# Performance work log

Measured on AMD Instinct MI355X. Metric: run time of the kernel, lower is better.

Reference implementation:

```python
import jax, jax.numpy as jnp
import numpy as np

VOCAB, EMB, HID = 50000, 256, 512
N, T = 256, 512


def setup_inputs() -> dict:
    key = jax.random.key(0)
    ks = jax.random.split(key, 9)
    s_ih = 1.0 / np.sqrt(HID)
    return {
        "input1": jax.random.randint(ks[0], (N, T), 0, VOCAB, dtype=jnp.int32),
        "input2": jax.random.randint(ks[1], (N, T), 0, VOCAB, dtype=jnp.int32),
        "emb_table": jax.random.normal(ks[2], (VOCAB, EMB), jnp.float32),
        "W_ih": jax.random.normal(ks[3], (4 * HID, EMB), jnp.float32) * s_ih,
        "W_hh": jax.random.normal(ks[4], (4 * HID, HID), jnp.float32) * s_ih,
        "b_ih": jax.random.normal(ks[5], (4 * HID,), jnp.float32) * s_ih,
        "b_hh": jax.random.normal(ks[6], (4 * HID,), jnp.float32) * s_ih,
        "W_fc": jax.random.normal(ks[7], (2, HID), jnp.float32) * s_ih,
        "b_fc": jax.random.normal(ks[8], (2,), jnp.float32) * s_ih,
    }


def _lstm_last_h(tokens, emb_table, W_ih, W_hh, b):
    # tokens: [N, T] int -> embedded [N, T, E]
    x = emb_table[tokens]
    # precompute input projections for all timesteps: [T, N, 4H]
    xg = jnp.einsum("nte,ge->tng", x, W_ih) + b
    h0 = jnp.zeros((tokens.shape[0], HID), x.dtype)
    c0 = jnp.zeros_like(h0)

    def step(carry, xg_t):
        h, c = carry
        gates = xg_t + h @ W_hh.T  # [N, 4H]
        i, f, g, o = jnp.split(gates, 4, axis=-1)
        i, f, o = jax.nn.sigmoid(i), jax.nn.sigmoid(f), jax.nn.sigmoid(o)
        g = jnp.tanh(g)
        c = f * c + i * g
        h = o * jnp.tanh(c)
        return (h, c), None

    (h, _), _ = jax.lax.scan(step, (h0, c0), xg)
    return h  # [N, HID]


def reference(input1, input2, emb_table, W_ih, W_hh, b_ih, b_hh, W_fc, b_fc):
    b = b_ih + b_hh
    h1 = _lstm_last_h(input1, emb_table, W_ih, W_hh, b)
    h2 = _lstm_last_h(input2, emb_table, W_ih, W_hh, b)
    h = h1 * h2  # combo_unit == 'MULT'
    logits = h @ W_fc.T + b_fc  # [N, 2]
    return jax.nn.softmax(logits, axis=1)
```

## Files before the change

kernel.cpp:

```cpp
#include <hip/hip_runtime.h>
#include <stdint.h>

#define VOCAB  50000
#define EMBD   256
#define HIDD   512
#define G4     2048
#define NBAT   256
#define TSEQ   512

#define O_P2    0ull
#define O_EMBT  204800000ull
#define O_WIH   230400000ull
#define O_WHH   231448576ull
#define O_TOKT  233545728ull
#define O_HBUF  234594304ull
#define O_BAR   235642880ull
#define WS_NEED 235643136ull
#define O_FLAGS O_EMBT

typedef __bf16 bf16x8 __attribute__((ext_vector_type(8)));
typedef float  f32x4  __attribute__((ext_vector_type(4)));
typedef float  f32x16 __attribute__((ext_vector_type(16)));

__device__ __forceinline__ unsigned short f2bf(float x) {
  unsigned u = __float_as_uint(x);
  u = (u + 0x7fffu + ((u >> 16) & 1u)) >> 16;
  return (unsigned short)u;
}
__device__ __forceinline__ float b2f(unsigned short b) {
  return __uint_as_float(((unsigned)b) << 16);
}
__device__ __forceinline__ float sigf(float x) {
  float e = __builtin_amdgcn_exp2f(-1.4426950408889634f * x);
  return __builtin_amdgcn_rcpf(1.0f + e);
}
__device__ __forceinline__ float tanhf_(float x) {
  float e = __builtin_amdgcn_exp2f(-2.8853900817779268f * x);
  return 2.0f * __builtin_amdgcn_rcpf(1.0f + e) - 1.0f;
}

__global__ void k_prep(const float* __restrict__ emb, const float* __restrict__ wih,
                       const float* __restrict__ whh, const int* __restrict__ tok1,
                       const int* __restrict__ tok2, unsigned short* __restrict__ embT,
                       unsigned short* __restrict__ wihb, unsigned short* __restrict__ whhb,
                       int* __restrict__ tokT, unsigned* __restrict__ hz)
{
  const int stride = gridDim.x * blockDim.x;
  const int id0 = blockIdx.x * blockDim.x + threadIdx.x;
  for (int i = id0; i < VOCAB * EMBD; i += stride) embT[i] = f2bf(emb[i]);
  for (int i = id0; i < G4 * EMBD; i += stride)    wihb[i] = f2bf(wih[i]);
  for (int i = id0; i < G4 * HIDD; i += stride)    whhb[i] = f2bf(whh[i]);
  for (int i = id0; i < 2 * TSEQ * NBAT; i += stride) {
    int l = i >> 17, t = (i >> 8) & 511, n = i & 255;
    tokT[i] = (l ? tok2 : tok1)[n * TSEQ + t];
  }
  for (int i = id0; i < 262144; i += stride) hz[i] = 0u;
}

__global__ void k_zero(unsigned* __restrict__ flags)
{
  const int i = blockIdx.x * blockDim.x + threadIdx.x;
  if (i < 16384) flags[i] = 0u;
}

__global__ __launch_bounds__(256) void
k_proj(const unsigned short* __restrict__ embT, const unsigned short* __restrict__ wihb,
       const float* __restrict__ bih, const float* __restrict__ bhh,
       unsigned short* __restrict__ P2)
{
  const int l  = threadIdx.x & 63;
  const int w  = threadIdx.x >> 6;
  const int n0 = blockIdx.x * 128 + (w & 1) * 64;
  const int m0 = blockIdx.y * 128 + (w >> 1) * 64;
  const int lq = l >> 4, lc = l & 15;

  f32x4 acc[4][4];
  #pragma unroll
  for (int a = 0; a < 4; ++a)
    #pragma unroll
    for (int b = 0; b < 4; ++b) acc[a][b] = (f32x4){0.f, 0.f, 0.f, 0.f};

  const uint8_t* eb = (const uint8_t*)embT;
  const uint8_t* wb = (const uint8_t*)wihb;
  #pragma unroll
  for (int ks = 0; ks < 8; ++ks) {
    const int koff = ks * 64 + lq * 16;
    bf16x8 a[4], b[4];
    #pragma unroll
    for (int mt = 0; mt < 4; ++mt) {
      int row = m0 + mt * 16 + lc; if (row >= VOCAB) row = VOCAB - 1;
      a[mt] = *(const bf16x8*)(eb + (size_t)row * 512 + koff);
    }
    #pragma unroll
    for (int nt = 0; nt < 4; ++nt) {
      int g = n0 + nt * 16 + lc;
      b[nt] = *(const bf16x8*)(wb + (size_t)g * 512 + koff);
    }
    #pragma unroll
    for (int mt = 0; mt < 4; ++mt)
      #pragma unroll
      for (int nt = 0; nt < 4; ++nt)
        acc[mt][nt] = __builtin_amdgcn_mfma_f32_16x16x32_bf16(a[mt], b[nt], acc[mt][nt], 0, 0, 0);
  }

  #pragma unroll
  for (int mt = 0; mt < 4; ++mt)
    #pragma unroll
    for (int r = 0; r < 4; ++r) {
      const int vrow = m0 + mt * 16 + lq * 4 + r;
      if (vrow < VOCAB) {
        #pragma unroll
        for (int nt = 0; nt < 4; ++nt) {
          const int gcol = n0 + nt * 16 + lc;
          float v = acc[mt][nt][r] + bih[gcol] + bhh[gcol];
          const int colp = ((gcol & 511) << 2) | (gcol >> 9);
          P2[(size_t)vrow * 2048 + colp] = f2bf(v);
        }
      }
    }
}

#define GB 32768

__global__ __launch_bounds__(256, 1) void
k_lstm(const uint8_t* __restrict__ P2, const int* __restrict__ tokT,
       const uint8_t* __restrict__ whh, uint8_t* __restrict__ hbuf,
       unsigned* __restrict__ flags)
{
  __shared__ __align__(16) uint8_t smem[163840];
  const int tid  = threadIdx.x;
  const int l    = tid & 63;
  const int w    = tid >> 6;
  const int bid  = blockIdx.x;
  const int jb   = bid & 15;
  const int mg   = (bid >> 4) & 7;
  const int lstm = bid >> 7;
  const int grp  = bid >> 4;
  const int m0   = mg * 32;
  const int j0   = jb * 32;

  const size_t hslot = (size_t)NBAT * HIDD * 2;
  const int em   = tid >> 3;
  const int ecol = tid & 7;
  const int an   = l & 31;
  const int ah   = l >> 5;

  bf16x8 wreg[32];
  {
    const uint8_t* wrow = whh + (size_t)(w * 512 + j0 + an) * 1024 + (size_t)ah * 16;
    #pragma unroll
    for (int ks = 0; ks < 32; ++ks)
      wreg[ks] = *(const bf16x8*)(wrow + ks * 32);
  }

  const unsigned* fpoll = flags + (size_t)(grp * 16 + (l & 15)) * 64;
  unsigned* fmine = flags + (size_t)bid * 64;

  float cst[4] = {0.f, 0.f, 0.f, 0.f};
  int tok_next = tokT[(lstm * TSEQ + 0) * NBAT + m0 + em];

  for (int t = 0; t < TSEQ; ++t) {
    const int tok_cur = tok_next;

    const uint8_t* xsrc = P2 + (size_t)tok_cur * 4096 + (size_t)j0 * 8 + (size_t)ecol * 32;
    const uint4 xq0 = *(const uint4*)(xsrc);
    const uint4 xq1 = *(const uint4*)(xsrc + 16);
    if (t + 1 < TSEQ) tok_next = tokT[(lstm * TSEQ + (t + 1)) * NBAT + m0 + em];

    if (t > 0 && w == 0) {
      const unsigned tgt = (unsigned)t;
      int guard = 0;
      for (;;) {
        const unsigned v = __hip_atomic_load(fpoll, __ATOMIC_RELAXED, __HIP_MEMORY_SCOPE_AGENT);
        if (__all((int)(v >= tgt))) break;
        __builtin_amdgcn_s_sleep(1);
        if (++guard > 400000) break;
      }
    }
    __syncthreads();

    {
      const uint8_t* hb = hbuf + (size_t)(lstm * 2 + (t & 1)) * hslot
                        + (size_t)m0 * 1024 + (size_t)tid * 8;
      unsigned long long v[16];
      #pragma unroll
      for (int i = 0; i < 16; ++i)
        v[i] = __hip_atomic_load((const unsigned long long*)(hb + (size_t)i * 2048),
                                 __ATOMIC_RELAXED, __HIP_MEMORY_SCOPE_AGENT);
      #pragma unroll
      for (int i = 0; i < 16; ++i) {
        const int m = i * 2 + (tid >> 7);
        const int c = (tid >> 1) & 63;
        const int half = tid & 1;
        *(unsigned long long*)(smem + (size_t)m * 1024
                               + ((c ^ (m & 7)) * 16) + half * 8) = v[i];
      }
    }
    __syncthreads();

    f32x16 acc0{}, acc1{};
    #pragma unroll
    for (int ks = 0; ks < 32; ++ks) {
      const int ch = ks * 2 + ah;
      const bf16x8 av = *(const bf16x8*)(smem + (size_t)an * 1024 + ((ch ^ (an & 7)) * 16));
      if (ks & 1) acc1 = __builtin_amdgcn_mfma_f32_32x32x16_bf16(av, wreg[ks], acc1, 0, 0, 0);
      else        acc0 = __builtin_amdgcn_mfma_f32_32x32x16_bf16(av, wreg[ks], acc0, 0, 0, 0);
    }

    {
      float* gb = (float*)(smem + GB);
      #pragma unroll
      for (int r = 0; r < 16; ++r) {
        const int row = (r & 3) + 8 * (r >> 2) + 4 * ah;
        gb[w * 1024 + row * 32 + an] = acc0[r] + acc1[r];
      }
    }
    __syncthreads();

    {
      const float* gb = (const float*)(smem + GB);
      const f32x4 pi = *(const f32x4*)(gb + 0 * 1024 + em * 32 + ecol * 4);
      const f32x4 pf = *(const f32x4*)(gb + 1 * 1024 + em * 32 + ecol * 4);
      const f32x4 pg = *(const f32x4*)(gb + 2 * 1024 + em * 32 + ecol * 4);
      const f32x4 po = *(const f32x4*)(gb + 3 * 1024 + em * 32 + ecol * 4);
      unsigned short xsv[16];
      *(uint4*)(xsv) = xq0;
      *(uint4*)(xsv + 8) = xq1;
      unsigned short hv[4];
      #pragma unroll
      for (int k = 0; k < 4; ++k) {
        const float iv = sigf(pi[k] + b2f(xsv[k * 4 + 0]));
        const float fv = sigf(pf[k] + b2f(xsv[k * 4 + 1]));
        const float gv = tanhf_(pg[k] + b2f(xsv[k * 4 + 2]));
        const float ov = sigf(po[k] + b2f(xsv[k * 4 + 3]));
        const float cv = fv * cst[k] + iv * gv;
        cst[k] = cv;
        hv[k] = f2bf(ov * tanhf_(cv));
      }
      unsigned long long hp =
          (unsigned long long)hv[0] | ((unsigned long long)hv[1] << 16) |
          ((unsigned long long)hv[2] << 32) | ((unsigned long long)hv[3] << 48);
      uint8_t* hdst = hbuf + (size_t)(lstm * 2 + ((t + 1) & 1)) * hslot
                    + (size_t)(m0 + em) * 1024 + (size_t)(j0 + ecol * 4) * 2;
      __hip_atomic_store((unsigned long long*)hdst, hp,
                         __ATOMIC_RELAXED, __HIP_MEMORY_SCOPE_AGENT);
    }
    __syncthreads();

    if (tid == 0 && t + 1 < TSEQ)
      __hip_atomic_store(fmine, (unsigned)(t + 1),
                         __ATOMIC_RELAXED, __HIP_MEMORY_SCOPE_AGENT);
  }
}

__global__ __launch_bounds__(64) void
k_fc(const uint8_t* __restrict__ hbuf, const float* __restrict__ wfc,
     const float* __restrict__ bfc, float* __restrict__ out)
{
  const int n = blockIdx.x, l = threadIdx.x;
  const unsigned short* h1 = (const unsigned short*)(hbuf) + (size_t)n * HIDD;
  const unsigned short* h2 = (const unsigned short*)(hbuf + 2 * (size_t)NBAT * HIDD * 2) + (size_t)n * HIDD;
  float s0 = 0.f, s1 = 0.f;
  for (int j = l; j < HIDD; j += 64) {
    float hv = b2f(h1[j]) * b2f(h2[j]);
    s0 += hv * wfc[j];
    s1 += hv * wfc[HIDD + j];
  }
  #pragma unroll
  for (int off = 32; off > 0; off >>= 1) {
    s0 += __shfl_down(s0, off, 64);
    s1 += __shfl_down(s1, off, 64);
  }
  if (l == 0) {
    s0 += bfc[0]; s1 += bfc[1];
    float m  = fmaxf(s0, s1);
    float e0 = __builtin_amdgcn_exp2f((s0 - m) * 1.4426950408889634f);
    float e1 = __builtin_amdgcn_exp2f((s1 - m) * 1.4426950408889634f);
    float inv = 1.0f / (e0 + e1);
    out[n * 2 + 0] = e0 * inv;
    out[n * 2 + 1] = e1 * inv;
  }
}

extern "C" void kernel_launch(void* const* d_in, const int* in_sizes, int n_in,
                              void* d_out, int out_size, void* d_ws, size_t ws_size,
                              hipStream_t stream) {
  (void)in_sizes; (void)n_in; (void)out_size;
  if (ws_size < WS_NEED) return;

  const int*   tok1 = (const int*)d_in[0];
  const int*   tok2 = (const int*)d_in[1];
  const float* emb  = (const float*)d_in[2];
  const float* wih  = (const float*)d_in[3];
  const float* whh  = (const float*)d_in[4];
  const float* bih  = (const float*)d_in[5];
  const float* bhh  = (const float*)d_in[6];
  const float* wfc  = (const float*)d_in[7];
  const float* bfc  = (const float*)d_in[8];
  float* out = (float*)d_out;

  uint8_t* ws = (uint8_t*)d_ws;
  unsigned short* P2    = (unsigned short*)(ws + O_P2);
  unsigned short* embT  = (unsigned short*)(ws + O_EMBT);
  unsigned short* wihb  = (unsigned short*)(ws + O_WIH);
  unsigned short* whhb  = (unsigned short*)(ws + O_WHH);
  int*            tokT  = (int*)(ws + O_TOKT);
  uint8_t*        hbuf  = ws + O_HBUF;
  unsigned*       flags = (unsigned*)(ws + O_FLAGS);

  k_prep<<<1024, 256, 0, stream>>>(emb, wih, whh, tok1, tok2, embT, wihb, whhb,
                                   tokT, (unsigned*)hbuf);
  k_proj<<<dim3(16, 391), 256, 0, stream>>>(embT, wihb, bih, bhh, P2);
  k_zero<<<64, 256, 0, stream>>>(flags);

  {
    const uint8_t* p2p = (const uint8_t*)P2;
    const int*     tkp = tokT;
    const uint8_t* whp = (const uint8_t*)whhb;
    uint8_t*       hbp = hbuf;
    unsigned*      flp = flags;
    void* args[5] = {(void*)&p2p, (void*)&tkp, (void*)&whp, (void*)&hbp, (void*)&flp};
    hipError_t e = hipLaunchCooperativeKernel((void*)k_lstm, dim3(256), dim3(256),
                                              args, 0, stream);
    if (e != hipSuccess) {
      (void)hipGetLastError();
      k_lstm<<<256, 256, 0, stream>>>(p2p, tkp, whp, hbp, flp);
    }
  }

  k_fc<<<256, 64, 0, stream>>>(hbuf, wfc, bfc, out);
}
```

Measured before the change: 1.957 ms.

## Replace per-block flag barrier with tagged hidden-state words for sync

Each hidden-state pair is now stored with the step number in its upper 32 bits. Consumers spin on the data itself until every tag matches the current step, which replaces the separate flag polling, its extra __syncthreads, and the flag store. This is meant to remove the flag round trip and barrier latency on the critical path of every recurrent step. In exchange it doubles hidden-state traffic and makes all 256 threads poll global memory. The fc kernel and the zeroing kernel are adapted to the new packed layout.

```diff
diff --git a/kernel.cpp b/kernel.cpp
--- a/kernel.cpp
+++ b/kernel.cpp
@@ -14,13 +14,13 @@
 #define O_WHH   231448576ull
 #define O_TOKT  233545728ull
 #define O_HBUF  234594304ull
-#define O_BAR   235642880ull
 #define WS_NEED 235643136ull
-#define O_FLAGS O_EMBT
+#define O_HB2   O_EMBT
 
 typedef __bf16 bf16x8 __attribute__((ext_vector_type(8)));
 typedef float  f32x4  __attribute__((ext_vector_type(4)));
 typedef float  f32x16 __attribute__((ext_vector_type(16)));
+typedef unsigned long long u64;
 
 __device__ __forceinline__ unsigned short f2bf(float x) {
   unsigned u = __float_as_uint(x);
@@ -43,7 +43,7 @@
                        const float* __restrict__ whh, const int* __restrict__ tok1,
                        const int* __restrict__ tok2, unsigned short* __restrict__ embT,
                        unsigned short* __restrict__ wihb, unsigned short* __restrict__ whhb,
-                       int* __restrict__ tokT, unsigned* __restrict__ hz)
+                       int* __restrict__ tokT)
 {
   const int stride = gridDim.x * blockDim.x;
   const int id0 = blockIdx.x * blockDim.x + threadIdx.x;
@@ -54,13 +54,13 @@
     int l = i >> 17, t = (i >> 8) & 511, n = i & 255;
     tokT[i] = (l ? tok2 : tok1)[n * TSEQ + t];
   }
-  for (int i = id0; i < 262144; i += stride) hz[i] = 0u;
-}
-
-__global__ void k_zero(unsigned* __restrict__ flags)
-{
-  const int i = blockIdx.x * blockDim.x + threadIdx.x;
-  if (i < 16384) flags[i] = 0u;
+}
+
+__global__ void k_zero(u64* __restrict__ hb)
+{
+  const int stride = gridDim.x * blockDim.x;
+  for (int i = blockIdx.x * blockDim.x + threadIdx.x; i < 262144; i += stride)
+    hb[i] = 0ull;
 }
 
 __global__ __launch_bounds__(256) void
@@ -124,8 +124,7 @@
 
 __global__ __launch_bounds__(256, 1) void
 k_lstm(const uint8_t* __restrict__ P2, const int* __restrict__ tokT,
-       const uint8_t* __restrict__ whh, uint8_t* __restrict__ hbuf,
-       unsigned* __restrict__ flags)
+       const uint8_t* __restrict__ whh, uint8_t* __restrict__ hb2)
 {
   __shared__ __align__(16) uint8_t smem[163840];
   const int tid  = threadIdx.x;
@@ -135,11 +134,10 @@
   const int jb   = bid & 15;
   const int mg   = (bid >> 4) & 7;
   const int lstm = bid >> 7;
-  const int grp  = bid >> 4;
   const int m0   = mg * 32;
   const int j0   = jb * 32;
 
-  const size_t hslot = (size_t)NBAT * HIDD * 2;
+  const size_t pslot = 524288;
   const int em   = tid >> 3;
   const int ecol = tid & 7;
   const int an   = l & 31;
@@ -153,9 +151,6 @@
       wreg[ks] = *(const bf16x8*)(wrow + ks * 32);
   }
 
-  const unsigned* fpoll = flags + (size_t)(grp * 16 + (l & 15)) * 64;
-  unsigned* fmine = flags + (size_t)bid * 64;
-
   float cst[4] = {0.f, 0.f, 0.f, 0.f};
   int tok_next = tokT[(lstm * TSEQ + 0) * NBAT + m0 + em];
 
@@ -167,33 +162,34 @@
     const uint4 xq1 = *(const uint4*)(xsrc + 16);
     if (t + 1 < TSEQ) tok_next = tokT[(lstm * TSEQ + (t + 1)) * NBAT + m0 + em];
 
-    if (t > 0 && w == 0) {
+    u64 pk[32];
+    {
+      const uint8_t* hb = hb2 + (size_t)(lstm * 2 + (t & 1)) * pslot
+                        + (size_t)(m0 + (tid >> 7)) * 2048 + (size_t)(tid & 127) * 16;
       const unsigned tgt = (unsigned)t;
       int guard = 0;
       for (;;) {
-        const unsigned v = __hip_atomic_load(fpoll, __ATOMIC_RELAXED, __HIP_MEMORY_SCOPE_AGENT);
-        if (__all((int)(v >= tgt))) break;
+        #pragma unroll
+        for (int i = 0; i < 16; ++i) {
+          pk[2 * i]     = __hip_atomic_load((const u64*)(hb + (size_t)i * 4096),
+                                            __ATOMIC_RELAXED, __HIP_MEMORY_SCOPE_AGENT);
+          pk[2 * i + 1] = __hip_atomic_load((const u64*)(hb + (size_t)i * 4096 + 8),
+                                            __ATOMIC_RELAXED, __HIP_MEMORY_SCOPE_AGENT);
+        }
+        unsigned bad = 0;
+        #pragma unroll
+        for (int i = 0; i < 32; ++i) bad |= ((unsigned)(pk[i] >> 32)) ^ tgt;
+        if (bad == 0) break;
         __builtin_amdgcn_s_sleep(1);
-        if (++guard > 400000) break;
-      }
-    }
-    __syncthreads();
-
-    {
-      const uint8_t* hb = hbuf + (size_t)(lstm * 2 + (t & 1)) * hslot
-                        + (size_t)m0 * 1024 + (size_t)tid * 8;
-      unsigned long long v[16];
-      #pragma unroll
-      for (int i = 0; i < 16; ++i)
-        v[i] = __hip_atomic_load((const unsigned long long*)(hb + (size_t)i * 2048),
-                                 __ATOMIC_RELAXED, __HIP_MEMORY_SCOPE_AGENT);
+        if (++guard > 200000) break;
+      }
+      const int half = tid & 1;
+      const int c    = (tid >> 1) & 63;
       #pragma unroll
       for (int i = 0; i < 16; ++i) {
         const int m = i * 2 + (tid >> 7);
-        const int c = (tid >> 1) & 63;
-        const int half = tid & 1;
-        *(unsigned long long*)(smem + (size_t)m * 1024
-                               + ((c ^ (m & 7)) * 16) + half * 8) = v[i];
+        const u64 v = (pk[2 * i] & 0xffffffffull) | ((pk[2 * i + 1] & 0xffffffffull) << 32);
+        *(u64*)(smem + (size_t)m * 1024 + ((c ^ (m & 7)) * 16) + half * 8) = v;
       }
     }
     __syncthreads();
@@ -237,34 +233,31 @@
         cst[k] = cv;
         hv[k] = f2bf(ov * tanhf_(cv));
       }
-      unsigned long long hp =
-          (unsigned long long)hv[0] | ((unsigned long long)hv[1] << 16) |
-          ((unsigned long long)hv[2] << 32) | ((unsigned long long)hv[3] << 48);
-      uint8_t* hdst = hbuf + (size_t)(lstm * 2 + ((t + 1) & 1)) * hslot
-                    + (size_t)(m0 + em) * 1024 + (size_t)(j0 + ecol * 4) * 2;
-      __hip_atomic_store((unsigned long long*)hdst, hp,
-                         __ATOMIC_RELAXED, __HIP_MEMORY_SCOPE_AGENT);
-    }
-    __syncthreads();
-
-    if (tid == 0 && t + 1 < TSEQ)
-      __hip_atomic_store(fmine, (unsigned)(t + 1),
-                         __ATOMIC_RELAXED, __HIP_MEMORY_SCOPE_AGENT);
+      const u64 tagw = ((u64)(unsigned)(t + 1)) << 32;
+      const u64 p0 = (u64)hv[0] | ((u64)hv[1] << 16) | tagw;
+      const u64 p1 = (u64)hv[2] | ((u64)hv[3] << 16) | tagw;
+      uint8_t* hdst = hb2 + (size_t)(lstm * 2 + ((t + 1) & 1)) * pslot
+                    + (size_t)(m0 + em) * 2048 + (size_t)(j0 + ecol * 4) * 4;
+      __hip_atomic_store((u64*)hdst, p0, __ATOMIC_RELAXED, __HIP_MEMORY_SCOPE_AGENT);
+      __hip_atomic_store((u64*)(hdst + 8), p1, __ATOMIC_RELAXED, __HIP_MEMORY_SCOPE_AGENT);
+    }
   }
 }
 
 __global__ __launch_bounds__(64) void
-k_fc(const uint8_t* __restrict__ hbuf, const float* __restrict__ wfc,
+k_fc(const uint8_t* __restrict__ hb2, const float* __restrict__ wfc,
      const float* __restrict__ bfc, float* __restrict__ out)
 {
   const int n = blockIdx.x, l = threadIdx.x;
-  const unsigned short* h1 = (const unsigned short*)(hbuf) + (size_t)n * HIDD;
-  const unsigned short* h2 = (const unsigned short*)(hbuf + 2 * (size_t)NBAT * HIDD * 2) + (size_t)n * HIDD;
+  const u64* h1 = (const u64*)(hb2 + (size_t)n * 2048);
+  const u64* h2 = (const u64*)(hb2 + 2 * 524288ull + (size_t)n * 2048);
   float s0 = 0.f, s1 = 0.f;
-  for (int j = l; j < HIDD; j += 64) {
-    float hv = b2f(h1[j]) * b2f(h2[j]);
-    s0 += hv * wfc[j];
-    s1 += hv * wfc[HIDD + j];
+  for (int p = l; p < 256; p += 64) {
+    const u64 k1 = h1[p], k2 = h2[p];
+    const float a0 = b2f((unsigned short)k1) * b2f((unsigned short)k2);
+    const float a1 = b2f((unsigned short)(k1 >> 16)) * b2f((unsigned short)(k2 >> 16));
+    s0 += a0 * wfc[2 * p]     + a1 * wfc[2 * p + 1];
+    s1 += a0 * wfc[HIDD + 2 * p] + a1 * wfc[HIDD + 2 * p + 1];
   }
   #pragma unroll
   for (int off = 32; off > 0; off >>= 1) {
@@ -305,28 +298,25 @@
   unsigned short* wihb  = (unsigned short*)(ws + O_WIH);
   unsigned short* whhb  = (unsigned short*)(ws + O_WHH);
   int*            tokT  = (int*)(ws + O_TOKT);
-  uint8_t*        hbuf  = ws + O_HBUF;
-  unsigned*       flags = (unsigned*)(ws + O_FLAGS);
-
-  k_prep<<<1024, 256, 0, stream>>>(emb, wih, whh, tok1, tok2, embT, wihb, whhb,
-                                   tokT, (unsigned*)hbuf);
+  uint8_t*        hb2   = ws + O_HB2;
+
+  k_prep<<<1024, 256, 0, stream>>>(emb, wih, whh, tok1, tok2, embT, wihb, whhb, tokT);
   k_proj<<<dim3(16, 391), 256, 0, stream>>>(embT, wihb, bih, bhh, P2);
-  k_zero<<<64, 256, 0, stream>>>(flags);
+  k_zero<<<1024, 256, 0, stream>>>((u64*)hb2);
 
   {
     const uint8_t* p2p = (const uint8_t*)P2;
     const int*     tkp = tokT;
     const uint8_t* whp = (const uint8_t*)whhb;
-    uint8_t*       hbp = hbuf;
-    unsigned*      flp = flags;
-    void* args[5] = {(void*)&p2p, (void*)&tkp, (void*)&whp, (void*)&hbp, (void*)&flp};
+    uint8_t*       hbp = hb2;
+    void* args[4] = {(void*)&p2p, (void*)&tkp, (void*)&whp, (void*)&hbp};
     hipError_t e = hipLaunchCooperativeKernel((void*)k_lstm, dim3(256), dim3(256),
                                               args, 0, stream);
     if (e != hipSuccess) {
       (void)hipGetLastError();
-      k_lstm<<<256, 256, 0, stream>>>(p2p, tkp, whp, hbp, flp);
-    }
-  }
-
-  k_fc<<<256, 64, 0, stream>>>(hbuf, wfc, bfc, out);
-}
+      k_lstm<<<256, 256, 0, stream>>>(p2p, tkp, whp, hbp);
+    }
+  }
+
+  k_fc<<<256, 64, 0, stream>>>(hb2, wfc, bfc, out);
+}
```

New measurement: 2.797 ms. 1.43x slower.
